# Performance work log

Hardware: AMD Instinct MI355X
Metric: run time of the kernel (lower is better)

## Reference

```python
import jax, jax.numpy as jnp
import numpy as np

N_SEQ, N_RES, C_M = 512, 384, 256
C_OUTER, C_Z = 32, 128
LN_EPS = 1e-5
EPS = 1e-3


def setup_inputs() -> dict:
    key = jax.random.key(0)
    ks = jax.random.split(key, 8)
    act = jax.random.normal(ks[0], (N_SEQ, N_RES, C_M), dtype=jnp.float32)
    # binary MSA mask (float, as used multiplicatively in the module)
    mask = (jax.random.uniform(ks[1], (N_SEQ, N_RES)) < 0.9).astype(jnp.float32)
    s = 1.0 / np.sqrt(C_M)
    left_w = jax.random.normal(ks[2], (C_M, C_OUTER), dtype=jnp.float32) * s
    left_b = jnp.zeros((C_OUTER,), dtype=jnp.float32)
    right_w = jax.random.normal(ks[3], (C_M, C_OUTER), dtype=jnp.float32) * s
    right_b = jnp.zeros((C_OUTER,), dtype=jnp.float32)
    # zero_init=False -> VarianceScaling(scale=2.0, fan_in=C_OUTER*C_OUTER)
    ow_s = np.sqrt(2.0 / (C_OUTER * C_OUTER))
    output_w = jax.random.normal(ks[4], (C_OUTER, C_OUTER, C_Z), dtype=jnp.float32) * ow_s
    output_b = jnp.zeros((C_Z,), dtype=jnp.float32)
    ln_scale = jnp.ones((C_M,), dtype=jnp.float32)
    ln_offset = jnp.zeros((C_M,), dtype=jnp.float32)
    return {
        "act": act, "mask": mask,
        "ln_scale": ln_scale, "ln_offset": ln_offset,
        "left_w": left_w, "left_b": left_b,
        "right_w": right_w, "right_b": right_b,
        "output_w": output_w, "output_b": output_b,
    }


def reference(act, mask, ln_scale, ln_offset, left_w, left_b, right_w, right_b, output_w, output_b):
    # act: [N_seq, N_res, c_m], mask: [N_seq, N_res]
    m = mask[..., None]
    mu = jnp.mean(act, axis=-1, keepdims=True)
    var = jnp.var(act, axis=-1, keepdims=True)
    act_n = (act - mu) * jax.lax.rsqrt(var + LN_EPS) * ln_scale + ln_offset
    left = m * (jnp.einsum('abm,mc->abc', act_n, left_w) + left_b)    # [a, b, c]
    right = m * (jnp.einsum('adm,me->ade', act_n, right_w) + right_b)  # [a, d, e]
    # outer product mean over sequence dim a: [b, d, c, e]
    inter = jnp.einsum('abc,ade->bdce', left, right)
    out = jnp.einsum('bdce,cef->bdf', inter, output_w) + output_b      # [b, d, f]
    norm = jnp.einsum('ab,ad->bd', mask, mask)[..., None]              # [b, d, 1]
    return out / (EPS + norm)
```

## Files before the change

### kernel.cpp

```cpp
#include <hip/hip_runtime.h>

#define N_SEQ 512
#define N_RES 384
#define C_M   256

typedef __bf16 bf16;
typedef __bf16 bf16x4 __attribute__((ext_vector_type(4)));
typedef __bf16 bf16x8 __attribute__((ext_vector_type(8)));
typedef float  f32x4  __attribute__((ext_vector_type(4)));
typedef float  f32x16 __attribute__((ext_vector_type(16)));

static __device__ __forceinline__ bf16x8 ld8(const bf16* p) {
  bf16x4 lo = *(const bf16x4*)p;
  bf16x4 hi = *(const bf16x4*)(p + 4);
  bf16x8 r;
  r[0] = lo[0]; r[1] = lo[1]; r[2] = lo[2]; r[3] = lo[3];
  r[4] = hi[0]; r[5] = hi[1]; r[6] = hi[2]; r[7] = hi[3];
  return r;
}

template <int N> __device__ __forceinline__ void wait_vm() {
  __builtin_amdgcn_s_waitcnt((N & 15) | ((N >> 4) << 14) | (7 << 4) | (15 << 8));
}


__global__ void aux_kernel(const float* __restrict__ mask,
                           const float* __restrict__ lw, const float* __restrict__ rw,
                           const float* __restrict__ ow,
                           const float* __restrict__ ln_scale, const float* __restrict__ ln_offset,
                           const float* __restrict__ left_b, const float* __restrict__ right_b,
                           bf16* __restrict__ projW2, bf16* __restrict__ WtEp,
                           float* __restrict__ Svec, float* __restrict__ bias2,
                           float* __restrict__ recip) {
  int blk = blockIdx.x, t = threadIdx.x;
  if (blk < 576) {
    int bx = blk % 24, by = blk / 24;
    int b = bx * 16 + (t & 15), d = by * 16 + (t >> 4);
    float s = 0.f;
#pragma unroll 8
    for (int a = 0; a < N_SEQ; ++a)
      s += mask[a * N_RES + b] * mask[a * N_RES + d];
    recip[b * N_RES + d] = 1.0f / (1e-3f + s);
  } else if (blk < 1088) {
    int i2 = (blk - 576) * 256 + t;
    int f = i2 >> 10, k = i2 & 1023, e = k >> 5, c = k & 31;
    WtEp[i2] = (bf16)ow[(c * 32 + e) * 128 + f];
  } else if (blk < 1152) {
    int idx = (blk - 1088) * 256 + t;
    int o = idx >> 8, m = idx & 255;
    float w = (o < 32) ? lw[m * 32 + o] : rw[m * 32 + (o - 32)];
    projW2[idx] = (bf16)(ln_scale[m] * w);
  } else {
    if (t < 64) {
      int o = t;
      float s = 0.f, b2 = (o < 32) ? left_b[o] : right_b[o - 32];
      for (int m = 0; m < 256; ++m) {
        float w = (o < 32) ? lw[m * 32 + o] : rw[m * 32 + (o - 32)];
        s += (float)(bf16)(ln_scale[m] * w);
        b2 += ln_offset[m] * w;
      }
      Svec[o] = s; bias2[o] = b2;
    }
  }
}

__launch_bounds__(256)
__global__ void ln_project_kernel(const float* __restrict__ act, const float* __restrict__ mask,
                                  const bf16* __restrict__ projW2,
                                  const float* __restrict__ Svec, const float* __restrict__ bias2,
                                  bf16* __restrict__ leftT, bf16* __restrict__ rightT) {
  __shared__ __align__(16) bf16 At[128 * 264];
  __shared__ float2 muRow[128];
  bf16* outbuf = At;

  const int t = threadIdx.x;
  const int b = blockIdx.y;
  const int a0 = blockIdx.x * 128;
  const int wv = t >> 6, lane = t & 63;
  const int q = lane >> 4, l15 = lane & 15;

#pragma unroll 4
  for (int it = 0; it < 32; ++it) {
    const int row = it * 4 + wv;
    float4 v = *(const float4*)(act + ((size_t)(a0 + row) * N_RES + b) * C_M + lane * 4);
    bf16x4 r;
    r[0] = (bf16)v.x; r[1] = (bf16)v.y; r[2] = (bf16)v.z; r[3] = (bf16)v.w;
    *(bf16x4*)&At[row * 264 + lane * 4] = r;
  }
  __syncthreads();

  {
    int row = t >> 1, half = t & 1;
    const bf16* base = At + row * 264 + half * 128;
    float s1 = 0.f, s2 = 0.f;
#pragma unroll
    for (int i = 0; i < 16; ++i) {
      int ch = ((i + row) & 15) * 8;
      bf16x8 v = *(const bf16x8*)(base + ch);
#pragma unroll
      for (int u = 0; u < 8; ++u) { float x = (float)v[u]; s1 += x; s2 += x * x; }
    }
    s1 += __shfl_xor(s1, 1);
    s2 += __shfl_xor(s2, 1);
    if (half == 0) {
      float mean = s1 * (1.f / 256.f);
      float var  = s2 * (1.f / 256.f) - mean * mean;
      muRow[row] = make_float2(mean, rsqrtf(var + 1e-5f));
    }
  }

  f32x4 acc[2][4] = {};
#pragma unroll
  for (int s = 0; s < 8; ++s) {
    bf16x8 af[2], bfr[4];
#pragma unroll
    for (int i = 0; i < 2; ++i)
      af[i] = *(bf16x8*)&At[(wv * 32 + i * 16 + l15) * 264 + s * 32 + q * 8];
#pragma unroll
    for (int j = 0; j < 4; ++j)
      bfr[j] = *(const bf16x8*)&projW2[(j * 16 + l15) * 256 + s * 32 + q * 8];
#pragma unroll
    for (int i = 0; i < 2; ++i)
#pragma unroll
      for (int j = 0; j < 4; ++j)
        acc[i][j] = __builtin_amdgcn_mfma_f32_16x16x32_bf16(af[i], bfr[j], acc[i][j], 0, 0, 0);
  }
  __syncthreads();

  float Sv[4], Bv[4];
#pragma unroll
  for (int j = 0; j < 4; ++j) { Sv[j] = Svec[j * 16 + l15]; Bv[j] = bias2[j * 16 + l15]; }
#pragma unroll
  for (int i = 0; i < 2; ++i) {
#pragma unroll
    for (int r = 0; r < 4; ++r) {
      int a_local = wv * 32 + i * 16 + q * 4 + r;
      float2 ms = muRow[a_local];
      float mv = mask[(size_t)(a0 + a_local) * N_RES + b];
#pragma unroll
      for (int j = 0; j < 4; ++j) {
        float val = (ms.y * (acc[i][j][r] - ms.x * Sv[j]) + Bv[j]) * mv;
        outbuf[(j * 16 + l15) * 136 + a_local] = (bf16)val;
      }
    }
  }
  __syncthreads();

  {
    int o = t >> 2, part = t & 3;
    bf16* dst = (o < 32) ? (leftT + (size_t)(b * 32 + o) * 512)
                         : (rightT + (size_t)(b * 32 + (o - 32)) * 512);
#pragma unroll
    for (int v = 0; v < 4; ++v) {
      int asub = part * 32 + v * 8;
      bf16x8 val = *(bf16x8*)&outbuf[o * 136 + asub];
      *(bf16x8*)(dst + a0 + asub) = val;
    }
  }
}

__launch_bounds__(512, 2)
__global__ void outer_kernel(const bf16* __restrict__ leftT, const bf16* __restrict__ rightT,
                             const bf16* __restrict__ WtEp, const float* __restrict__ output_b,
                             const float* __restrict__ recip, float* __restrict__ out) {
  __shared__ __align__(16) union {
    bf16 AB[8 * 8192];
    bf16 Aep[64 * 1156];
    float P[4 * 64 * 2 * 64];
  } sm;

  const int t_ = threadIdx.x;
  const int sq = blockIdx.x >> 4, wi = blockIdx.x & 15;
  const int m0 = ((sq % 12) * 4 + (wi & 3)) * 256;
  const int n0 = ((sq / 12) * 4 + (wi >> 2)) * 256;

  const int wv = t_ >> 6, lane = t_ & 63;
  const int q = lane >> 4, l15 = lane & 15;
  const int l31 = lane & 31, h = lane >> 5;
  const int wm = (wv & 1) * 128, wn = (wv >> 1) * 64;

  const int stR  = wv * 32 + (lane >> 2);
  const int stKC = ((lane & 3) ^ ((lane >> 3) & 3)) * 8;
  const int rsw  = (l31 >> 1) & 3;

  const bf16* gA = leftT  + (size_t)m0 * 512;
  const bf16* gB = rightT + (size_t)n0 * 512;

#define BLK(d, mat, hf) ((((d) * 2 + (mat)) * 2 + (hf)) * 8192)
#define STAGE(mat, T, hf) do {                                                              \
    const bf16* _g = (mat) ? gB : gA;                                                       \
    bf16* _l = sm.AB + BLK((T) & 1, mat, hf);                                               \
    _Pragma("unroll")                                                                       \
    for (int _j = 0; _j < 2; ++_j) {                                                        \
      const bf16* _s = _g + (size_t)(stR + _j * 16) * 512 + (T) * 64 + (hf) * 32 + stKC;    \
      __builtin_amdgcn_global_load_lds(                                                     \
          (const __attribute__((address_space(1))) void*)_s,                                \
          (__attribute__((address_space(3))) void*)(_l + (wv * 2 + _j) * 512), 16, 0, 0);   \
    }                                                                                       \
  } while (0)

  f32x16 acc[4][2] = {};

  STAGE(0, 0, 0); STAGE(1, 0, 0);
  STAGE(0, 0, 1); STAGE(1, 0, 1);
  STAGE(0, 1, 0); STAGE(1, 1, 0);
  wait_vm<8>();
  __builtin_amdgcn_s_barrier();

#pragma unroll
  for (int t = 0; t < 8; ++t) {
#pragma unroll
    for (int s = 0; s < 4; ++s) {
      const bf16* Ab = sm.AB + BLK(t & 1, 0, s >> 1);
      const bf16* Bb = sm.AB + BLK(t & 1, 1, s >> 1);
      const int coff = (((s & 1) * 2 + h) ^ rsw) * 8;
      bf16x8 af[4], b0, b1;
#pragma unroll
      for (int i = 0; i < 4; ++i)
        af[i] = *(const bf16x8*)&Ab[(wm + i * 32 + l31) * 32 + coff];
      b0 = *(const bf16x8*)&Bb[(wn + l31) * 32 + coff];
      b1 = *(const bf16x8*)&Bb[(wn + 32 + l31) * 32 + coff];

      if (s == 1) { if (t < 7) wait_vm<6>(); else wait_vm<0>(); }
      if (s == 3) { if (t < 6) wait_vm<6>(); else if (t == 6) wait_vm<4>(); }

      __builtin_amdgcn_s_barrier();

      if (s == 0) { if (t < 7) STAGE(0, t + 1, 1); }
      if (s == 1) { if (t < 7) STAGE(1, t + 1, 1); }
      if (s == 2) { if (t < 6) STAGE(0, t + 2, 0); }
      if (s == 3) { if (t < 6) STAGE(1, t + 2, 0); }

      __builtin_amdgcn_s_setprio(1);
#pragma unroll
      for (int i = 0; i < 4; ++i) {
        acc[i][0] = __builtin_amdgcn_mfma_f32_32x32x16_bf16(af[i], b0, acc[i][0], 0, 0, 0);
        acc[i][1] = __builtin_amdgcn_mfma_f32_32x32x16_bf16(af[i], b1, acc[i][1], 0, 0, 0);
      }
      __builtin_amdgcn_s_setprio(0);
      __builtin_amdgcn_s_barrier();
    }
  }
  __syncthreads();

#pragma unroll
  for (int i = 0; i < 4; ++i) {
#pragma unroll
    for (int j = 0; j < 2; ++j) {
      int pair = ((wv & 1) * 4 + i) * 8 + (wv >> 1) * 2 + j;
      int base = pair * 1156 + l31 * 36;
#pragma unroll
      for (int g = 0; g < 4; ++g) {
        bf16x4 v;
        v[0] = (bf16)acc[i][j][4 * g + 0];
        v[1] = (bf16)acc[i][j][4 * g + 1];
        v[2] = (bf16)acc[i][j][4 * g + 2];
        v[3] = (bf16)acc[i][j][4 * g + 3];
        *(bf16x4*)&sm.Aep[base + 8 * g + 4 * h] = v;
      }
    }
  }
  __syncthreads();

  const int kq = wv & 3, fh = wv >> 2;
  f32x4 eacc[4][4] = {};
#pragma unroll
  for (int si = 0; si < 8; ++si) {
    int e = kq * 8 + si;
    bf16x8 wf[4];
#pragma unroll
    for (int j = 0; j < 4; ++j)
      wf[j] = *(const bf16x8*)&WtEp[(size_t)(fh * 64 + j * 16 + l15) * 1024 + e * 32 + q * 8];
    bf16x8 af[4];
#pragma unroll
    for (int mt = 0; mt < 4; ++mt)
      af[mt] = ld8(&sm.Aep[(mt * 16 + l15) * 1156 + e * 36 + q * 8]);
#pragma unroll
    for (int mt = 0; mt < 4; ++mt)
#pragma unroll
      for (int j = 0; j < 4; ++j)
        eacc[mt][j] = __builtin_amdgcn_mfma_f32_16x16x32_bf16(af[mt], wf[j], eacc[mt][j], 0, 0, 0);
  }
  __syncthreads();

#pragma unroll
  for (int mt = 0; mt < 4; ++mt)
#pragma unroll
    for (int j = 0; j < 4; ++j)
#pragma unroll
      for (int r = 0; r < 4; ++r) {
        int pair = mt * 16 + q * 4 + r;
        int fl = j * 16 + l15;
        sm.P[((kq * 64 + pair) * 2 + fh) * 64 + fl] = eacc[mt][j][r];
      }
  __syncthreads();

#pragma unroll
  for (int gg = 0; gg < 4; ++gg) {
    int g = t_ + 512 * gg;
    int pair = g >> 5, f4 = g & 31;
    int f = f4 * 4, fh2 = f >> 6, fl = f & 63;
    f32x4 s = {};
#pragma unroll
    for (int k2 = 0; k2 < 4; ++k2)
      s += *(f32x4*)&sm.P[((k2 * 64 + pair) * 2 + fh2) * 64 + fl];
    int b = (m0 >> 5) + (pair >> 3);
    int d = (n0 >> 5) + (pair & 7);
    float rc = recip[b * N_RES + d];
    float4 ob = *(const float4*)(output_b + f);
    f32x4 o;
    o[0] = (s[0] + ob.x) * rc; o[1] = (s[1] + ob.y) * rc;
    o[2] = (s[2] + ob.z) * rc; o[3] = (s[3] + ob.w) * rc;
    *(f32x4*)(out + ((size_t)b * N_RES + d) * 128 + f) = o;
  }
}

extern "C" void kernel_launch(void* const* d_in, const int* in_sizes, int n_in,
                              void* d_out, int out_size, void* d_ws, size_t ws_size,
                              hipStream_t stream) {
  const float* act       = (const float*)d_in[0];
  const float* mask      = (const float*)d_in[1];
  const float* ln_scale  = (const float*)d_in[2];
  const float* ln_offset = (const float*)d_in[3];
  const float* left_w    = (const float*)d_in[4];
  const float* left_b    = (const float*)d_in[5];
  const float* right_w   = (const float*)d_in[6];
  const float* right_b   = (const float*)d_in[7];
  const float* output_w  = (const float*)d_in[8];
  const float* output_b  = (const float*)d_in[9];
  float* out = (float*)d_out;

  char* ws = (char*)d_ws;
  bf16* leftT   = (bf16*)(ws);
  bf16* rightT  = (bf16*)(ws + 12582912);
  bf16* WtEp    = (bf16*)(ws + 25165824);
  bf16* projW2  = (bf16*)(ws + 25427968);
  float* Svec   = (float*)(ws + 25460736);
  float* bias2  = (float*)(ws + 25460992);
  float* recip  = (float*)(ws + 25461248);

  hipLaunchKernelGGL(aux_kernel, dim3(1153), dim3(256), 0, stream,
                     mask, left_w, right_w, output_w, ln_scale, ln_offset,
                     left_b, right_b, projW2, WtEp, Svec, bias2, recip);
  hipLaunchKernelGGL(ln_project_kernel, dim3(4, 384), dim3(256), 0, stream,
                     act, mask, projW2, Svec, bias2, leftT, rightT);
  hipLaunchKernelGGL(outer_kernel, dim3(2304), dim3(512), 0, stream,
                     leftT, rightT, WtEp, output_b, recip, out);
}
```

Measured before the change: 578.8 us.

## Halve outer GEMM N-tile, load B fragments directly from global, raise occupancy

The outer-product GEMM tile shrinks from 256x256 to 256x128 and the grid doubles. Only the A operand is now staged into LDS through async global-to-LDS loads. B fragments are read straight from global memory into registers inside the k-loop. Launch bounds go from 2 to 4 blocks per CU to hide latency with more waves. The risk is lower data reuse per tile and per-iteration global loads for B that may stall the MFMA stream.

```diff
diff --git a/kernel.cpp b/kernel.cpp
--- a/kernel.cpp
+++ b/kernel.cpp
@@ -159,25 +159,25 @@
   }
 }
 
-__launch_bounds__(512, 2)
+__launch_bounds__(512, 4)
 __global__ void outer_kernel(const bf16* __restrict__ leftT, const bf16* __restrict__ rightT,
                              const bf16* __restrict__ WtEp, const float* __restrict__ output_b,
                              const float* __restrict__ recip, float* __restrict__ out) {
   __shared__ __align__(16) union {
-    bf16 AB[8 * 8192];
-    bf16 Aep[64 * 1156];
-    float P[4 * 64 * 2 * 64];
+    bf16 A[4 * 8192];
+    bf16 Aep[32 * 1156];
+    float P[4 * 32 * 2 * 64];
   } sm;
 
   const int t_ = threadIdx.x;
-  const int sq = blockIdx.x >> 4, wi = blockIdx.x & 15;
+  const int sq = blockIdx.x >> 5, wi = blockIdx.x & 31;
   const int m0 = ((sq % 12) * 4 + (wi & 3)) * 256;
-  const int n0 = ((sq / 12) * 4 + (wi >> 2)) * 256;
+  const int n0 = ((sq / 12) * 8 + (wi >> 2)) * 128;
 
   const int wv = t_ >> 6, lane = t_ & 63;
   const int q = lane >> 4, l15 = lane & 15;
   const int l31 = lane & 31, h = lane >> 5;
-  const int wm = (wv & 1) * 128, wn = (wv >> 1) * 64;
+  const int wm = (wv >> 1) * 64, wn = (wv & 1) * 64;
 
   const int stR  = wv * 32 + (lane >> 2);
   const int stKC = ((lane & 3) ^ ((lane >> 3) & 3)) * 8;
@@ -186,68 +186,61 @@
   const bf16* gA = leftT  + (size_t)m0 * 512;
   const bf16* gB = rightT + (size_t)n0 * 512;
 
-#define BLK(d, mat, hf) ((((d) * 2 + (mat)) * 2 + (hf)) * 8192)
-#define STAGE(mat, T, hf) do {                                                              \
-    const bf16* _g = (mat) ? gB : gA;                                                       \
-    bf16* _l = sm.AB + BLK((T) & 1, mat, hf);                                               \
+#define ABLK(par, hf) (((par) * 2 + (hf)) * 8192)
+#define STAGE(T, hf) do {                                                                   \
+    bf16* _l = sm.A + ABLK((T) & 1, hf);                                                    \
     _Pragma("unroll")                                                                       \
     for (int _j = 0; _j < 2; ++_j) {                                                        \
-      const bf16* _s = _g + (size_t)(stR + _j * 16) * 512 + (T) * 64 + (hf) * 32 + stKC;    \
+      const bf16* _s = gA + (size_t)(stR + _j * 16) * 512 + (T) * 64 + (hf) * 32 + stKC;    \
       __builtin_amdgcn_global_load_lds(                                                     \
           (const __attribute__((address_space(1))) void*)_s,                                \
           (__attribute__((address_space(3))) void*)(_l + (wv * 2 + _j) * 512), 16, 0, 0);   \
     }                                                                                       \
   } while (0)
 
-  f32x16 acc[4][2] = {};
-
-  STAGE(0, 0, 0); STAGE(1, 0, 0);
-  STAGE(0, 0, 1); STAGE(1, 0, 1);
-  STAGE(0, 1, 0); STAGE(1, 1, 0);
-  wait_vm<8>();
-  __builtin_amdgcn_s_barrier();
+  f32x16 acc[2][2] = {};
+
+  STAGE(0, 0);
+  STAGE(0, 1);
+  STAGE(1, 0);
+  wait_vm<4>();
 
 #pragma unroll
   for (int t = 0; t < 8; ++t) {
 #pragma unroll
     for (int s = 0; s < 4; ++s) {
-      const bf16* Ab = sm.AB + BLK(t & 1, 0, s >> 1);
-      const bf16* Bb = sm.AB + BLK(t & 1, 1, s >> 1);
+      __builtin_amdgcn_s_barrier();
+
+      const bf16* Ab = sm.A + ABLK(t & 1, s >> 1);
       const int coff = (((s & 1) * 2 + h) ^ rsw) * 8;
-      bf16x8 af[4], b0, b1;
-#pragma unroll
-      for (int i = 0; i < 4; ++i)
-        af[i] = *(const bf16x8*)&Ab[(wm + i * 32 + l31) * 32 + coff];
-      b0 = *(const bf16x8*)&Bb[(wn + l31) * 32 + coff];
-      b1 = *(const bf16x8*)&Bb[(wn + 32 + l31) * 32 + coff];
-
-      if (s == 1) { if (t < 7) wait_vm<6>(); else wait_vm<0>(); }
-      if (s == 3) { if (t < 6) wait_vm<6>(); else if (t == 6) wait_vm<4>(); }
-
-      __builtin_amdgcn_s_barrier();
-
-      if (s == 0) { if (t < 7) STAGE(0, t + 1, 1); }
-      if (s == 1) { if (t < 7) STAGE(1, t + 1, 1); }
-      if (s == 2) { if (t < 6) STAGE(0, t + 2, 0); }
-      if (s == 3) { if (t < 6) STAGE(1, t + 2, 0); }
+      bf16x8 af0 = *(const bf16x8*)&Ab[(wm + l31) * 32 + coff];
+      bf16x8 af1 = *(const bf16x8*)&Ab[(wm + 32 + l31) * 32 + coff];
+
+      const bf16* Bb = gB + (size_t)wn * 512 + t * 64 + s * 16 + h * 8;
+      bf16x8 b0 = *(const bf16x8*)(Bb + (size_t)l31 * 512);
+      bf16x8 b1 = *(const bf16x8*)(Bb + (size_t)(32 + l31) * 512);
 
       __builtin_amdgcn_s_setprio(1);
-#pragma unroll
-      for (int i = 0; i < 4; ++i) {
-        acc[i][0] = __builtin_amdgcn_mfma_f32_32x32x16_bf16(af[i], b0, acc[i][0], 0, 0, 0);
-        acc[i][1] = __builtin_amdgcn_mfma_f32_32x32x16_bf16(af[i], b1, acc[i][1], 0, 0, 0);
-      }
+      acc[0][0] = __builtin_amdgcn_mfma_f32_32x32x16_bf16(af0, b0, acc[0][0], 0, 0, 0);
+      acc[0][1] = __builtin_amdgcn_mfma_f32_32x32x16_bf16(af0, b1, acc[0][1], 0, 0, 0);
+      acc[1][0] = __builtin_amdgcn_mfma_f32_32x32x16_bf16(af1, b0, acc[1][0], 0, 0, 0);
+      acc[1][1] = __builtin_amdgcn_mfma_f32_32x32x16_bf16(af1, b1, acc[1][1], 0, 0, 0);
       __builtin_amdgcn_s_setprio(0);
-      __builtin_amdgcn_s_barrier();
-    }
-  }
-  __syncthreads();
-
-#pragma unroll
-  for (int i = 0; i < 4; ++i) {
+
+      if (s == 0) { if (t < 7) STAGE(t + 1, 1); }
+      if (s == 2) { if (t < 6) STAGE(t + 2, 0); }
+
+      if (s == 1) { if (t < 7) wait_vm<4>(); else wait_vm<0>(); }
+      if (s == 3) { if (t < 6) wait_vm<4>(); else if (t == 6) wait_vm<2>(); }
+    }
+  }
+  __syncthreads();
+
+#pragma unroll
+  for (int i = 0; i < 2; ++i) {
 #pragma unroll
     for (int j = 0; j < 2; ++j) {
-      int pair = ((wv & 1) * 4 + i) * 8 + (wv >> 1) * 2 + j;
+      int pair = ((wv >> 1) * 2 + i) * 4 + (wv & 1) * 2 + j;
       int base = pair * 1156 + l31 * 36;
 #pragma unroll
       for (int g = 0; g < 4; ++g) {
@@ -263,7 +256,7 @@
   __syncthreads();
 
   const int kq = wv & 3, fh = wv >> 2;
-  f32x4 eacc[4][4] = {};
+  f32x4 eacc[2][4] = {};
 #pragma unroll
   for (int si = 0; si < 8; ++si) {
     int e = kq * 8 + si;
@@ -271,12 +264,12 @@
 #pragma unroll
     for (int j = 0; j < 4; ++j)
       wf[j] = *(const bf16x8*)&WtEp[(size_t)(fh * 64 + j * 16 + l15) * 1024 + e * 32 + q * 8];
-    bf16x8 af[4];
-#pragma unroll
-    for (int mt = 0; mt < 4; ++mt)
+    bf16x8 af[2];
+#pragma unroll
+    for (int mt = 0; mt < 2; ++mt)
       af[mt] = ld8(&sm.Aep[(mt * 16 + l15) * 1156 + e * 36 + q * 8]);
 #pragma unroll
-    for (int mt = 0; mt < 4; ++mt)
+    for (int mt = 0; mt < 2; ++mt)
 #pragma unroll
       for (int j = 0; j < 4; ++j)
         eacc[mt][j] = __builtin_amdgcn_mfma_f32_16x16x32_bf16(af[mt], wf[j], eacc[mt][j], 0, 0, 0);
@@ -284,28 +277,28 @@
   __syncthreads();
 
 #pragma unroll
-  for (int mt = 0; mt < 4; ++mt)
+  for (int mt = 0; mt < 2; ++mt)
 #pragma unroll
     for (int j = 0; j < 4; ++j)
 #pragma unroll
       for (int r = 0; r < 4; ++r) {
         int pair = mt * 16 + q * 4 + r;
         int fl = j * 16 + l15;
-        sm.P[((kq * 64 + pair) * 2 + fh) * 64 + fl] = eacc[mt][j][r];
+        sm.P[((kq * 32 + pair) * 2 + fh) * 64 + fl] = eacc[mt][j][r];
       }
   __syncthreads();
 
 #pragma unroll
-  for (int gg = 0; gg < 4; ++gg) {
+  for (int gg = 0; gg < 2; ++gg) {
     int g = t_ + 512 * gg;
     int pair = g >> 5, f4 = g & 31;
     int f = f4 * 4, fh2 = f >> 6, fl = f & 63;
     f32x4 s = {};
 #pragma unroll
     for (int k2 = 0; k2 < 4; ++k2)
-      s += *(f32x4*)&sm.P[((k2 * 64 + pair) * 2 + fh2) * 64 + fl];
-    int b = (m0 >> 5) + (pair >> 3);
-    int d = (n0 >> 5) + (pair & 7);
+      s += *(f32x4*)&sm.P[((k2 * 32 + pair) * 2 + fh2) * 64 + fl];
+    int b = (m0 >> 5) + (pair >> 2);
+    int d = (n0 >> 5) + (pair & 3);
     float rc = recip[b * N_RES + d];
     float4 ob = *(const float4*)(output_b + f);
     f32x4 o;
@@ -344,6 +337,6 @@
                      left_b, right_b, projW2, WtEp, Svec, bias2, recip);
   hipLaunchKernelGGL(ln_project_kernel, dim3(4, 384), dim3(256), 0, stream,
                      act, mask, projW2, Svec, bias2, leftT, rightT);
-  hipLaunchKernelGGL(outer_kernel, dim3(2304), dim3(512), 0, stream,
+  hipLaunchKernelGGL(outer_kernel, dim3(4608), dim3(512), 0, stream,
                      leftT, rightT, WtEp, output_b, recip, out);
 }
```

After: 797.2 us. +37.7%, slower.
